# Performance work log

Measured on AMD Instinct MI355X. Metric: run time of the kernel, lower is better.

The kernel has to match this reference:

```python
import jax, jax.numpy as jnp
import numpy as np

HEADS = 8
DIM_HEAD = 64
MP_ADD_T = 0.3
EPS = 1e-4


def normalize_weight(w, eps=EPS):
    # Karras forced weight norm: per-output-channel L2 norm over all other dims
    dims = tuple(range(1, w.ndim))
    n = jnp.sqrt(jnp.sum(w * w, axis=dims, keepdims=True))
    alpha = np.sqrt(n.size / w.size)  # = 1/sqrt(fan_in)
    return w / (eps + alpha * n)


def pixel_norm(t, eps=EPS):
    # F.normalize(dim=-1) * sqrt(d): x / max(||x||, eps) * sqrt(d)
    n = jnp.sqrt(jnp.sum(t * t, axis=-1, keepdims=True))
    return t / jnp.maximum(n, eps) * np.sqrt(t.shape[-1])


def conv1x1(x, w):
    # x: [b,c,h,w], w: [o,c] (normalized weight / sqrt(fan_in))
    wn = normalize_weight(w) / np.sqrt(w.shape[1])  # fan_in = dim_in * 1 * 1
    return jnp.einsum('bchw,oc->bohw', x, wn)


def setup_inputs() -> dict:
    key = jax.random.key(0)
    k1, k2, k3, k4 = jax.random.split(key, 4)
    b, c, h, w = 16, 512, 32, 32
    hidden = HEADS * DIM_HEAD
    return {
        'x': jax.random.normal(k1, (b, c, h, w), dtype=jnp.float32),
        'w_qkv': jax.random.normal(k2, (hidden * 3, c), dtype=jnp.float32),
        'w_out': jax.random.normal(k3, (c, hidden), dtype=jnp.float32),
        'mem_kv': jax.random.normal(k4, (2, HEADS, 4, DIM_HEAD), dtype=jnp.float32),
    }


def reference(x, w_qkv, w_out, mem_kv):
    b, c, h, w = x.shape
    n = h * w
    qkv = conv1x1(x, w_qkv)  # [b, 3*hidden, h, w]
    q, k, v = jnp.split(qkv, 3, axis=1)

    def to_heads(t):
        # b (h c) x y -> b h (x y) c
        return t.reshape(b, HEADS, DIM_HEAD, n).transpose(0, 1, 3, 2)

    q, k, v = map(to_heads, (q, k, v))
    mk = jnp.broadcast_to(mem_kv[0], (b,) + mem_kv[0].shape)  # [b,h,m,d]
    mv = jnp.broadcast_to(mem_kv[1], (b,) + mem_kv[1].shape)
    k = jnp.concatenate([mk, k], axis=2)
    v = jnp.concatenate([mv, v], axis=2)

    q, k, v = map(pixel_norm, (q, k, v))

    sim = jnp.einsum('bhid,bhjd->bhij', q, k) * (DIM_HEAD ** -0.5)
    attn = jax.nn.softmax(sim, axis=-1)  # dropout is identity in eval
    out = jnp.einsum('bhij,bhjd->bhid', attn, v)  # [b,h,n,d]

    # b h (x y) d -> b (h d) x y
    out = out.transpose(0, 1, 3, 2).reshape(b, HEADS * DIM_HEAD, h, w)
    out = conv1x1(out, w_out)

    # MPAdd: magnitude-preserving residual
    t = MP_ADD_T
    den = np.sqrt((1 - t) ** 2 + t ** 2)
    return (out * (1.0 - t) + x * t) / den
```

## Files before the change

kernel.cpp:

```cpp
#include <hip/hip_runtime.h>
#include <hip/hip_bf16.h>
#include <math.h>

#define HEADS 8
#define DIMH 64
#define NPIX 1024
#define BATCH 16
#define CIN 512
#define HIDDEN 512
#define OQKV 1536

typedef __attribute__((ext_vector_type(8))) short v8s;
typedef __attribute__((ext_vector_type(4))) float v4f;
typedef __attribute__((ext_vector_type(4))) int v4i;

#define MFMA16(a, b, c) __builtin_amdgcn_mfma_f32_16x16x32_bf16(a, b, c, 0, 0, 0)

__device__ inline unsigned pkbf(float lo, float hi) {
    unsigned r;
    asm("v_cvt_pk_bf16_f32 %0, %1, %2" : "=v"(r) : "v"(lo), "v"(hi));
    return r;
}
__device__ inline ushort bf16u(float f) {
    __hip_bfloat16 h = __float2bfloat16(f);
    return *(ushort*)&h;
}
__device__ inline float exp2i(float x) {
    float r;
    asm("v_exp_f32 %0, %1" : "=v"(r) : "v"(x));
    return r;
}
__device__ inline float bf2f(ushort u) {
    return __uint_as_float(((unsigned)u) << 16);
}
__device__ inline void gload16(const ushort* g, ushort* l) {
    __builtin_amdgcn_global_load_lds(
        (const __attribute__((address_space(1))) void*)g,
        (__attribute__((address_space(3))) void*)l, 16, 0, 0);
}

#define INVLN2 1.44269504088896f
#define BIAS2  12.2629078475662f

__global__ __launch_bounds__(256) void prep_fused(
    const float* __restrict__ x,
    const float* __restrict__ wq, const float* __restrict__ wo,
    const float* __restrict__ mem_kv,
    ushort* __restrict__ Xt, ushort* __restrict__ wn,
    __hip_bfloat16* __restrict__ mk, __hip_bfloat16* __restrict__ mv,
    float* __restrict__ msk)
{
    int bid = blockIdx.x;
    if (bid < 2048) {
        int b = bid >> 7, rem = bid & 127;
        int c0 = (rem >> 4) * 64, p0 = (rem & 15) * 64;
        __shared__ ushort lds[64][72];
        int tid = threadIdx.x;
        int cl = tid >> 2;
        int pl = (tid & 3) * 16;
        const float* src = x + ((size_t)b * CIN + c0 + cl) * NPIX + p0 + pl;
        #pragma unroll
        for (int j = 0; j < 4; j++) {
            float4 v = *(const float4*)(src + j * 4);
            lds[cl][pl + j * 4 + 0] = bf16u(v.x);
            lds[cl][pl + j * 4 + 1] = bf16u(v.y);
            lds[cl][pl + j * 4 + 2] = bf16u(v.z);
            lds[cl][pl + j * 4 + 3] = bf16u(v.w);
        }
        __syncthreads();
        int pw = tid >> 2;
        int cs = (tid & 3) * 16;
        union { ushort u[16]; uint4 q[2]; } tmp;
        #pragma unroll
        for (int j = 0; j < 16; j++) tmp.u[j] = lds[cs + j][pw];
        ushort* dst = Xt + ((size_t)b * NPIX + p0 + pw) * CIN + c0 + cs;
        *(uint4*)(dst) = tmp.q[0];
        *(uint4*)(dst + 8) = tmp.q[1];
    } else if (bid < 4096) {
        int row = bid - 2048;
        const float* src = (row < OQKV) ? (wq + (size_t)row * CIN)
                                        : (wo + (size_t)(row - OQKV) * CIN);
        int t = threadIdx.x;
        float v0 = src[t];
        float v1 = src[t + 256];
        float ss = v0 * v0 + v1 * v1;
        #pragma unroll
        for (int off = 32; off >= 1; off >>= 1) ss += __shfl_xor(ss, off);
        __shared__ float red[4];
        if ((t & 63) == 0) red[t >> 6] = ss;
        __syncthreads();
        float total = red[0] + red[1] + red[2] + red[3];
        const float RSQRT512 = 0.044194173824159216f;
        const float SQRT512  = 22.627416997969522f;
        float scale = 1.0f / ((1e-4f + sqrtf(total) * RSQRT512) * SQRT512);
        ushort* dst = wn + (size_t)row * CIN;
        dst[t] = bf16u(v0 * scale);
        dst[t + 256] = bf16u(v1 * scale);
    } else {
        if (threadIdx.x < 64) {
            int h = bid - 4096;
            int lane = threadIdx.x;
            #pragma unroll
            for (int m = 0; m < 4; m++) {
                float kvv = mem_kv[((size_t)h * 4 + m) * 64 + lane];
                float vvv = mem_kv[((size_t)(HEADS + h) * 4 + m) * 64 + lane];
                float ssk = kvv * kvv, ssv = vvv * vvv;
                #pragma unroll
                for (int off = 32; off >= 1; off >>= 1) {
                    ssk += __shfl_xor(ssk, off);
                    ssv += __shfl_xor(ssv, off);
                }
                float sck = 8.0f / fmaxf(sqrtf(ssk), 1e-4f);
                float scv = 8.0f / fmaxf(sqrtf(ssv), 1e-4f);
                mk[((size_t)h * 16 + m) * 64 + lane] = __float2bfloat16(kvv);
                mv[((size_t)h * 64 + lane) * 32 + m] = __float2bfloat16(vvv * scv);
                if (lane == 0) { msk[h * 16 + m] = sck; }
            }
            #pragma unroll
            for (int m = 4; m < 16; m++)
                mk[((size_t)h * 16 + m) * 64 + lane] = __float2bfloat16(0.f);
            #pragma unroll
            for (int m = 4; m < 32; m++)
                mv[((size_t)h * 64 + lane) * 32 + m] = __float2bfloat16(0.f);
            if (lane >= 4 && lane < 16) msk[h * 16 + lane] = 0.f;
        }
    }
}

__global__ __launch_bounds__(256) void gemm_qkv_mfma(
    const ushort* __restrict__ Wall,
    const ushort* __restrict__ Xt,
    ushort* __restrict__ Qb, ushort* __restrict__ Kb, ushort* __restrict__ Vb,
    float* __restrict__ qsA)
{
    int bid = blockIdx.x;
    int xcd = bid & 7;
    int rest = bid >> 3;
    int bh2 = rest / 96;
    int r = rest - bh2 * 96;
    int b = xcd + (bh2 << 3);
    int yy = r % 12;
    int pp = r / 12;

    int p0 = pp * 128;
    int isV = (yy >= 8) ? 1 : 0;
    int o0 = (isV ? (yy - 8) : yy) * 128;
    const ushort* Wsrc = Wall + (isV ? (size_t)1024 * CIN : 0);

    int tid = threadIdx.x;
    int wave = tid >> 6, lane = tid & 63;
    int wy = wave >> 1, wx = wave & 1;
    int col = lane & 15, lg = lane >> 4;
    int pw = p0 + wx * 64;
    int ow = o0 + wy * 64;

    __shared__ __align__(16) ushort sW[128 * 64];
    __shared__ __align__(16) ushort sX[128 * 64];

    int rIn = lane >> 3;
    int chS = (lane & 7) ^ rIn;
    int rowStage = wave * 32 + rIn;
    const ushort* gW = Wsrc + (size_t)(o0 + rowStage) * CIN + chS * 8;
    const ushort* gX = Xt + ((size_t)b * NPIX + p0 + rowStage) * CIN + chS * 8;

    v4f acc[4][4];
    #pragma unroll
    for (int i = 0; i < 4; i++)
        #pragma unroll
        for (int j = 0; j < 4; j++) acc[i][j] = (v4f){0.f, 0.f, 0.f, 0.f};

    const ushort* sA = isV ? sX : sW;
    const ushort* sB = isV ? sW : sX;
    int rowA = (isV ? wx : wy) * 64 + col;
    int rowB = (isV ? wy : wx) * 64 + col;
    int c7 = col & 7;

    #pragma unroll 1
    for (int c0 = 0; c0 < CIN; c0 += 64) {
        #pragma unroll
        for (int j = 0; j < 4; j++) {
            gload16(gW + (size_t)j * 8 * CIN + c0, &sW[(wave * 4 + j) * 512]);
            gload16(gX + (size_t)j * 8 * CIN + c0, &sX[(wave * 4 + j) * 512]);
        }
        __syncthreads();
        #pragma unroll
        for (int hh = 0; hh < 2; hh++) {
            int ch = (hh * 4 + lg) ^ c7;
            v8s af[4], bf[4];
            #pragma unroll
            for (int i = 0; i < 4; i++) {
                af[i] = *(const v8s*)&sA[(rowA + i * 16) * 64 + ch * 8];
                bf[i] = *(const v8s*)&sB[(rowB + i * 16) * 64 + ch * 8];
            }
            #pragma unroll
            for (int i = 0; i < 4; i++)
                #pragma unroll
                for (int j = 0; j < 4; j++)
                    acc[i][j] = MFMA16(af[i], bf[j], acc[i][j]);
        }
        __syncthreads();
    }

    if (!isV) {
        int part = ow >> 9;
        int h = (ow >> 6) & 7;
        int bh = b * HEADS + h;

        float ssq[4];
        #pragma unroll
        for (int pt = 0; pt < 4; pt++) {
            float s = 0.f;
            #pragma unroll
            for (int dt = 0; dt < 4; dt++)
                #pragma unroll
                for (int r2 = 0; r2 < 4; r2++) s += acc[dt][pt][r2] * acc[dt][pt][r2];
            s += __shfl_xor(s, 16);
            s += __shfl_xor(s, 32);
            ssq[pt] = s;
        }
        if (part == 0) {
            if (lg == 0) {
                #pragma unroll
                for (int pt = 0; pt < 4; pt++)
                    qsA[(size_t)bh * NPIX + pw + pt * 16 + col] =
                        1.0f / fmaxf(sqrtf(ssq[pt]), 1e-4f);
            }
            ushort* dst = Qb + (size_t)bh * NPIX * DIMH;
            #pragma unroll
            for (int pt = 0; pt < 4; pt++) {
                int p = pw + pt * 16 + col;
                #pragma unroll
                for (int dt = 0; dt < 4; dt++) {
                    uint2 uu;
                    uu.x = pkbf(acc[dt][pt][0], acc[dt][pt][1]);
                    uu.y = pkbf(acc[dt][pt][2], acc[dt][pt][3]);
                    *(uint2*)(dst + (size_t)p * DIMH + dt * 16 + 4 * lg) = uu;
                }
            }
        } else {
            float scl[4];
            #pragma unroll
            for (int pt = 0; pt < 4; pt++)
                scl[pt] = 8.0f / fmaxf(sqrtf(ssq[pt]), 1e-4f);
            ushort* dst = Kb + (size_t)bh * NPIX * DIMH;
            #pragma unroll
            for (int pt = 0; pt < 4; pt++) {
                int p = pw + pt * 16 + col;
                #pragma unroll
                for (int dt = 0; dt < 4; dt++) {
                    uint2 uu;
                    uu.x = pkbf(acc[dt][pt][0] * scl[pt], acc[dt][pt][1] * scl[pt]);
                    uu.y = pkbf(acc[dt][pt][2] * scl[pt], acc[dt][pt][3] * scl[pt]);
                    *(uint2*)(dst + (size_t)p * DIMH + dt * 16 + 4 * lg) = uu;
                }
            }
        }
    } else {
        int h = (ow >> 6) & 7;
        int bh = b * HEADS + h;

        float scl[4][4];
        #pragma unroll
        for (int pt = 0; pt < 4; pt++) {
            #pragma unroll
            for (int r2 = 0; r2 < 4; r2++) {
                float s = acc[pt][0][r2] * acc[pt][0][r2] + acc[pt][1][r2] * acc[pt][1][r2]
                        + acc[pt][2][r2] * acc[pt][2][r2] + acc[pt][3][r2] * acc[pt][3][r2];
                s += __shfl_xor(s, 1);
                s += __shfl_xor(s, 2);
                s += __shfl_xor(s, 4);
                s += __shfl_xor(s, 8);
                scl[pt][r2] = 8.0f / fmaxf(sqrtf(s), 1e-4f);
            }
        }
        #pragma unroll
        for (int ot = 0; ot < 4; ot++) {
            int d = ot * 16 + col;
            #pragma unroll
            for (int pt = 0; pt < 4; pt++) {
                uint2 uu;
                uu.x = pkbf(acc[pt][ot][0] * scl[pt][0], acc[pt][ot][1] * scl[pt][1]);
                uu.y = pkbf(acc[pt][ot][2] * scl[pt][2], acc[pt][ot][3] * scl[pt][3]);
                *(uint2*)(Vb + ((size_t)bh * DIMH + d) * NPIX + pw + pt * 16 + 4 * lg) = uu;
            }
        }
    }
}

__global__ __launch_bounds__(256, 2) void attn_mfma_kernel(
    const __hip_bfloat16* __restrict__ Qb,
    const __hip_bfloat16* __restrict__ Kb,
    const __hip_bfloat16* __restrict__ Vb,
    const float* __restrict__ qsA,
    const __hip_bfloat16* __restrict__ mk, const __hip_bfloat16* __restrict__ mv,
    const float* __restrict__ msk,
    ushort* __restrict__ oP, float* __restrict__ lP)
{
    int bid = blockIdx.x;
    int ks = bid >> 9;
    int bh = bid & 127;
    int qb = (bid >> 7) & 3;
    int b = bh >> 3, h = bh & 7;
    int wave = threadIdx.x >> 6, lane = threadIdx.x & 63;
    int col = lane & 15, lg = lane >> 4;
    int q0 = qb * 256 + wave * 64;

    const __hip_bfloat16* Qbase = Qb + ((size_t)bh * NPIX + q0) * DIMH;
    const __hip_bfloat16* Kbase = Kb + ((size_t)bh * NPIX + ks * 512) * DIMH;
    const __hip_bfloat16* Vbase = Vb + (size_t)bh * DIMH * NPIX + ks * 512;

    v8s qf[4][2];
    float myqs[4];
    #pragma unroll
    for (int qt = 0; qt < 4; qt++) {
        #pragma unroll
        for (int dh = 0; dh < 2; dh++)
            qf[qt][dh] = *(const v8s*)(Qbase + (qt * 16 + col) * DIMH + dh * 32 + 8 * lg);
        myqs[qt] = qsA[(size_t)bh * NPIX + q0 + qt * 16 + col] * INVLN2;
    }

    v4f o_[4][4];
    #pragma unroll
    for (int qt = 0; qt < 4; qt++)
        #pragma unroll
        for (int dt = 0; dt < 4; dt++) o_[qt][dt] = (v4f){0.f, 0.f, 0.f, 0.f};
    float l_[4] = {0.f, 0.f, 0.f, 0.f};

    int srcA = ((lg & 1) << 5) + col;
    int srcB = srcA + 16;
    bool hig = (lg >= 2);

    if (ks == 0) {
        const __hip_bfloat16* mkh = mk + (size_t)h * 16 * DIMH;
        v8s kf0 = *(const v8s*)(mkh + col * DIMH + 8 * lg);
        v8s kf1 = *(const v8s*)(mkh + col * DIMH + 32 + 8 * lg);
        v8s vfm[4];
        #pragma unroll
        for (int dt = 0; dt < 4; dt++)
            vfm[dt] = *(const v8s*)(mv + ((size_t)h * DIMH + dt * 16 + col) * 32 + 8 * lg);
        float4 ksm = *(const float4*)&msk[h * 16 + 4 * lg];
        float ksr[4] = {ksm.x, ksm.y, ksm.z, ksm.w};

        #pragma unroll
        for (int qt = 0; qt < 4; qt++) {
            v4f c0 = (v4f){0.f, 0.f, 0.f, 0.f};
            c0 = MFMA16(kf0, qf[qt][0], c0);
            c0 = MFMA16(kf1, qf[qt][1], c0);
            float p0[4];
            #pragma unroll
            for (int r = 0; r < 4; r++) {
                float t = __builtin_fmaf(c0[r], myqs[qt] * ksr[r], -BIAS2);
                p0[r] = (lg == 0) ? exp2i(t) : 0.f;
                l_[qt] += p0[r];
            }
            unsigned A0 = pkbf(p0[0], p0[1]);
            unsigned A1 = pkbf(p0[2], p0[3]);
            int a0 = __shfl((int)A0, srcA), a1 = __shfl((int)A1, srcA);
            int a2 = __shfl((int)A0, srcB), a3 = __shfl((int)A1, srcB);
            v4i w;
            w.x = hig ? 0 : a0; w.y = hig ? 0 : a1;
            w.z = hig ? 0 : a2; w.w = hig ? 0 : a3;
            v8s pf = __builtin_bit_cast(v8s, w);
            #pragma unroll
            for (int dt = 0; dt < 4; dt++)
                o_[qt][dt] = MFMA16(vfm[dt], pf, o_[qt][dt]);
        }
    }

    v8s kfA[4], vfA[4], kfB[4], vfB[4];

    #define LOADK(dst, kk) { \
        const __hip_bfloat16* Kr = Kbase + (size_t)(kk) * DIMH; \
        dst[0] = *(const v8s*)(Kr + col * DIMH + 8 * lg); \
        dst[1] = *(const v8s*)(Kr + col * DIMH + 32 + 8 * lg); \
        dst[2] = *(const v8s*)(Kr + (16 + col) * DIMH + 8 * lg); \
        dst[3] = *(const v8s*)(Kr + (16 + col) * DIMH + 32 + 8 * lg); }
    #define LOADV(dst, kk) { \
        _Pragma("unroll") \
        for (int dt = 0; dt < 4; dt++) \
            dst[dt] = *(const v8s*)(Vbase + (size_t)(dt * 16 + col) * NPIX + (kk) + 8 * lg); }

    #define COMPUTE(kf, vf) { \
        _Pragma("unroll") \
        for (int qt = 0; qt < 4; qt++) { \
            v4f c0 = (v4f){0.f, 0.f, 0.f, 0.f}; \
            v4f c1 = (v4f){0.f, 0.f, 0.f, 0.f}; \
            __builtin_amdgcn_s_setprio(1); \
            c0 = MFMA16(kf[0], qf[qt][0], c0); \
            c0 = MFMA16(kf[1], qf[qt][1], c0); \
            c1 = MFMA16(kf[2], qf[qt][0], c1); \
            c1 = MFMA16(kf[3], qf[qt][1], c1); \
            __builtin_amdgcn_s_setprio(0); \
            float p0[4], p1[4]; \
            _Pragma("unroll") \
            for (int r = 0; r < 4; r++) { \
                p0[r] = exp2i(__builtin_fmaf(c0[r], myqs[qt], -BIAS2)); \
                p1[r] = exp2i(__builtin_fmaf(c1[r], myqs[qt], -BIAS2)); \
                l_[qt] += p0[r] + p1[r]; \
            } \
            unsigned A0 = pkbf(p0[0], p0[1]); \
            unsigned A1 = pkbf(p0[2], p0[3]); \
            unsigned B0 = pkbf(p1[0], p1[1]); \
            unsigned B1 = pkbf(p1[2], p1[3]); \
            int a0 = __shfl((int)A0, srcA), a1 = __shfl((int)A1, srcA); \
            int a2 = __shfl((int)A0, srcB), a3 = __shfl((int)A1, srcB); \
            int b0 = __shfl((int)B0, srcA), b1 = __shfl((int)B1, srcA); \
            int b2 = __shfl((int)B0, srcB), b3 = __shfl((int)B1, srcB); \
            v4i w; \
            w.x = hig ? b0 : a0; w.y = hig ? b1 : a1; \
            w.z = hig ? b2 : a2; w.w = hig ? b3 : a3; \
            v8s pf = __builtin_bit_cast(v8s, w); \
            __builtin_amdgcn_s_setprio(1); \
            _Pragma("unroll") \
            for (int dt = 0; dt < 4; dt++) \
                o_[qt][dt] = MFMA16(vf[dt], pf, o_[qt][dt]); \
            __builtin_amdgcn_s_setprio(0); \
        } }

    LOADK(kfA, 0);
    LOADV(vfA, 0);
    #pragma unroll 1
    for (int k0 = 0; k0 < 512; k0 += 64) {
        LOADK(kfB, k0 + 32);
        LOADV(vfB, k0 + 32);
        COMPUTE(kfA, vfA);
        LOADK(kfA, k0 + 64);
        LOADV(vfA, k0 + 64);
        COMPUTE(kfB, vfB);
    }

    #pragma unroll
    for (int qt = 0; qt < 4; qt++) {
        float l = l_[qt];
        l += __shfl_xor(l, 16);
        l += __shfl_xor(l, 32);
        int q = q0 + qt * 16 + col;
        if (lg == 0)
            lP[((size_t)ks * 128 + bh) * NPIX + q] = l;
        ushort* od = oP + (((size_t)ks * 128 + bh) * NPIX + q) * DIMH;
        #pragma unroll
        for (int dt = 0; dt < 4; dt++) {
            uint2 uu;
            uu.x = pkbf(o_[qt][dt][0], o_[qt][dt][1]);
            uu.y = pkbf(o_[qt][dt][2], o_[qt][dt][3]);
            *(uint2*)(od + dt * 16 + 4 * lg) = uu;
        }
    }
    #undef LOADK
    #undef LOADV
    #undef COMPUTE
}

__global__ __launch_bounds__(256) void attn_combine(
    const ushort* __restrict__ oP, const float* __restrict__ lP,
    ushort* __restrict__ attT)
{
    int gt = blockIdx.x * 256 + threadIdx.x;
    int rq = gt >> 3;
    int d0 = (gt & 7) * 8;
    int bh = rq >> 10, q = rq & 1023;
    float inv = 1.0f / (lP[rq] + lP[(size_t)128 * NPIX + rq]);
    const ushort* o0p = oP + (size_t)rq * DIMH + d0;
    const ushort* o1p = o0p + (size_t)128 * NPIX * DIMH;
    v8s a = *(const v8s*)o0p;
    v8s c = *(const v8s*)o1p;
    uint4 res;
    unsigned w[4];
    #pragma unroll
    for (int j = 0; j < 4; j++) {
        float lo = (bf2f(((ushort)a[2 * j]))     + bf2f(((ushort)c[2 * j])))     * inv;
        float hi = (bf2f(((ushort)a[2 * j + 1])) + bf2f(((ushort)c[2 * j + 1]))) * inv;
        w[j] = pkbf(lo, hi);
    }
    res.x = w[0]; res.y = w[1]; res.z = w[2]; res.w = w[3];
    int b = bh >> 3, h = bh & 7;
    *(uint4*)(attT + ((size_t)(b * NPIX + q)) * HIDDEN + h * DIMH + d0) = res;
}

__global__ __launch_bounds__(256) void gemm_out_mfma(
    const ushort* __restrict__ Wo,
    const ushort* __restrict__ attT,
    const float* __restrict__ x, float* __restrict__ out)
{
    int b = blockIdx.z;
    int o0 = blockIdx.y * 128;
    int p0 = blockIdx.x * 128;
    int tid = threadIdx.x;
    int wave = tid >> 6, lane = tid & 63;
    int wy = wave >> 1, wx = wave & 1;
    int col = lane & 15, lg = lane >> 4;
    int ow = o0 + wy * 64, pw = p0 + wx * 64;

    __shared__ __align__(16) ushort sAa[128 * 64];
    __shared__ __align__(16) ushort sBb[128 * 64];

    int rIn = lane >> 3;
    int chS = (lane & 7) ^ rIn;
    int rowStage = wave * 32 + rIn;
    const ushort* gA = attT + ((size_t)b * NPIX + p0 + rowStage) * HIDDEN + chS * 8;
    const ushort* gB = Wo + (size_t)(o0 + rowStage) * HIDDEN + chS * 8;

    v4f acc[4][4];
    #pragma unroll
    for (int i = 0; i < 4; i++)
        #pragma unroll
        for (int j = 0; j < 4; j++) acc[i][j] = (v4f){0.f, 0.f, 0.f, 0.f};

    int rowA = wx * 64 + col;
    int rowB = wy * 64 + col;
    int c7 = col & 7;

    #pragma unroll 1
    for (int c0 = 0; c0 < HIDDEN; c0 += 64) {
        #pragma unroll
        for (int j = 0; j < 4; j++) {
            gload16(gA + (size_t)j * 8 * HIDDEN + c0, &sAa[(wave * 4 + j) * 512]);
            gload16(gB + (size_t)j * 8 * HIDDEN + c0, &sBb[(wave * 4 + j) * 512]);
        }
        __syncthreads();
        #pragma unroll
        for (int hh = 0; hh < 2; hh++) {
            int ch = (hh * 4 + lg) ^ c7;
            v8s af[4], bf[4];
            #pragma unroll
            for (int i = 0; i < 4; i++) {
                af[i] = *(const v8s*)&sAa[(rowA + i * 16) * 64 + ch * 8];
                bf[i] = *(const v8s*)&sBb[(rowB + i * 16) * 64 + ch * 8];
            }
            #pragma unroll
            for (int i = 0; i < 4; i++)
                #pragma unroll
                for (int j = 0; j < 4; j++)
                    acc[i][j] = MFMA16(af[i], bf[j], acc[i][j]);
        }
        __syncthreads();
    }

    const float INV_DEN = 1.3130643285972254f;
    #pragma unroll
    for (int pt = 0; pt < 4; pt++) {
        #pragma unroll
        for (int ot = 0; ot < 4; ot++) {
            size_t base = ((size_t)b * HIDDEN + ow + ot * 16 + col) * NPIX
                        + pw + pt * 16 + 4 * lg;
            float4 res = *(const float4*)&x[base];
            float4 y;
            y.x = (acc[pt][ot][0] * 0.7f + res.x * 0.3f) * INV_DEN;
            y.y = (acc[pt][ot][1] * 0.7f + res.y * 0.3f) * INV_DEN;
            y.z = (acc[pt][ot][2] * 0.7f + res.z * 0.3f) * INV_DEN;
            y.w = (acc[pt][ot][3] * 0.7f + res.w * 0.3f) * INV_DEN;
            *(float4*)&out[base] = y;
        }
    }
}

extern "C" void kernel_launch(void* const* d_in, const int* in_sizes, int n_in,
                              void* d_out, int out_size, void* d_ws, size_t ws_size,
                              hipStream_t stream)
{
    const float* x      = (const float*)d_in[0];
    const float* w_qkv  = (const float*)d_in[1];
    const float* w_out  = (const float*)d_in[2];
    const float* mem_kv = (const float*)d_in[3];
    float* out = (float*)d_out;

    char* ws = (char*)d_ws;
    ushort* wnB = (ushort*)ws; ws += (size_t)2048 * CIN * 2;
    ushort* Xt  = (ushort*)ws; ws += (size_t)BATCH * NPIX * CIN * 2;
    ushort* Qb  = (ushort*)ws; ws += (size_t)BATCH * HEADS * NPIX * DIMH * 2;
    ushort* Kb  = (ushort*)ws; ws += (size_t)BATCH * HEADS * NPIX * DIMH * 2;
    ushort* Vb  = (ushort*)ws; ws += (size_t)BATCH * HEADS * NPIX * DIMH * 2;
    ushort* attT = (ushort*)ws; ws += (size_t)BATCH * NPIX * HIDDEN * 2;
    ushort* oP  = (ushort*)ws; ws += (size_t)2 * 128 * NPIX * DIMH * 2;
    float* lP  = (float*)ws;  ws += (size_t)2 * 128 * NPIX * 4;
    float* qsA = (float*)ws;  ws += (size_t)BATCH * HEADS * NPIX * 4;
    float* msk = (float*)ws;  ws += 8 * 16 * 4;
    __hip_bfloat16* mk = (__hip_bfloat16*)ws; ws += (size_t)8 * 16 * 64 * 2;
    __hip_bfloat16* mv = (__hip_bfloat16*)ws; ws += (size_t)8 * 64 * 32 * 2;

    prep_fused<<<4104, 256, 0, stream>>>(
        x, w_qkv, w_out, mem_kv, Xt, wnB, mk, mv, msk);

    gemm_qkv_mfma<<<1536, 256, 0, stream>>>(
        wnB, Xt, Qb, Kb, Vb, qsA);

    attn_mfma_kernel<<<1024, 256, 0, stream>>>(
        (const __hip_bfloat16*)Qb, (const __hip_bfloat16*)Kb,
        (const __hip_bfloat16*)Vb, qsA, mk, mv, msk, oP, lP);

    attn_combine<<<4096, 256, 0, stream>>>(oP, lP, attT);

    gemm_out_mfma<<<dim3(8, 4, BATCH), 256, 0, stream>>>(
        wnB + (size_t)OQKV * CIN, attT, x, out);
}
```

Baseline: 169.6 us.

## Stage K/V tiles through double-buffered swizzled LDS in attention kernel

Each wave previously loaded its own K and V fragments straight from global memory, so the four waves of a block fetched the same K/V data redundantly. Now the block cooperatively copies 64-key tiles of K and V into double-buffered shared memory with an XOR swizzle (via gload16, likely direct global-to-LDS) and prefetches the next tile while computing on the current one. This cuts global/L2 traffic by sharing tiles across waves, at the cost of 32KB of LDS per block, a block barrier per tile, and LDS read latency, which may limit occupancy.

```diff
diff --git a/kernel.cpp b/kernel.cpp
--- a/kernel.cpp
+++ b/kernel.cpp
@@ -305,9 +305,15 @@
     int col = lane & 15, lg = lane >> 4;
     int q0 = qb * 256 + wave * 64;
 
+    __shared__ __align__(16) ushort sK[2][64 * 64];
+    __shared__ __align__(16) ushort sV[2][64 * 64];
+
+    const ushort* Kg = (const ushort*)Kb + ((size_t)bh * NPIX + ks * 512) * DIMH;
+    const ushort* Vg = (const ushort*)Vb + (size_t)bh * DIMH * NPIX + ks * 512;
     const __hip_bfloat16* Qbase = Qb + ((size_t)bh * NPIX + q0) * DIMH;
-    const __hip_bfloat16* Kbase = Kb + ((size_t)bh * NPIX + ks * 512) * DIMH;
-    const __hip_bfloat16* Vbase = Vb + (size_t)bh * DIMH * NPIX + ks * 512;
+
+    int rIn = lane >> 3;
+    int chS = (lane & 7) ^ rIn;
 
     v8s qf[4][2];
     float myqs[4];
@@ -367,20 +373,26 @@
         }
     }
 
-    v8s kfA[4], vfA[4], kfB[4], vfB[4];
-
-    #define LOADK(dst, kk) { \
-        const __hip_bfloat16* Kr = Kbase + (size_t)(kk) * DIMH; \
-        dst[0] = *(const v8s*)(Kr + col * DIMH + 8 * lg); \
-        dst[1] = *(const v8s*)(Kr + col * DIMH + 32 + 8 * lg); \
-        dst[2] = *(const v8s*)(Kr + (16 + col) * DIMH + 8 * lg); \
-        dst[3] = *(const v8s*)(Kr + (16 + col) * DIMH + 32 + 8 * lg); }
-    #define LOADV(dst, kk) { \
+    #define STAGE(cur, kk) { \
+        _Pragma("unroll") \
+        for (int j = 0; j < 2; j++) { \
+            gload16(Kg + ((size_t)(kk) + wave * 16 + j * 8 + rIn) * 64 + chS * 8, \
+                    &sK[cur][wave * 1024 + j * 512]); \
+            gload16(Vg + ((size_t)(wave * 16 + j * 8 + rIn)) * 1024 + (kk) + chS * 8, \
+                    &sV[cur][wave * 1024 + j * 512]); \
+        } }
+
+    #define COMPUTE_LDS(cur, hs) { \
+        v8s kf[4], vf[4]; \
+        int rk0 = (hs) * 32 + col, rk1 = rk0 + 16; \
+        int sw = col & 7; \
+        kf[0] = *(const v8s*)&sK[cur][rk0 * 64 + ((lg    ) ^ sw) * 8]; \
+        kf[1] = *(const v8s*)&sK[cur][rk0 * 64 + ((lg + 4) ^ sw) * 8]; \
+        kf[2] = *(const v8s*)&sK[cur][rk1 * 64 + ((lg    ) ^ sw) * 8]; \
+        kf[3] = *(const v8s*)&sK[cur][rk1 * 64 + ((lg + 4) ^ sw) * 8]; \
         _Pragma("unroll") \
         for (int dt = 0; dt < 4; dt++) \
-            dst[dt] = *(const v8s*)(Vbase + (size_t)(dt * 16 + col) * NPIX + (kk) + 8 * lg); }
-
-    #define COMPUTE(kf, vf) { \
+            vf[dt] = *(const v8s*)&sV[cur][(dt * 16 + col) * 64 + (((hs) * 4 + lg) ^ sw) * 8]; \
         _Pragma("unroll") \
         for (int qt = 0; qt < 4; qt++) { \
             v4f c0 = (v4f){0.f, 0.f, 0.f, 0.f}; \
@@ -417,16 +429,16 @@
             __builtin_amdgcn_s_setprio(0); \
         } }
 
-    LOADK(kfA, 0);
-    LOADV(vfA, 0);
+    int cur = 0;
+    STAGE(0, 0);
+    __syncthreads();
     #pragma unroll 1
-    for (int k0 = 0; k0 < 512; k0 += 64) {
-        LOADK(kfB, k0 + 32);
-        LOADV(vfB, k0 + 32);
-        COMPUTE(kfA, vfA);
-        LOADK(kfA, k0 + 64);
-        LOADV(vfA, k0 + 64);
-        COMPUTE(kfB, vfB);
+    for (int t = 0; t < 8; t++) {
+        if (t < 7) STAGE(cur ^ 1, (t + 1) * 64);
+        COMPUTE_LDS(cur, 0);
+        COMPUTE_LDS(cur, 1);
+        __syncthreads();
+        cur ^= 1;
     }
 
     #pragma unroll
@@ -446,9 +458,8 @@
             *(uint2*)(od + dt * 16 + 4 * lg) = uu;
         }
     }
-    #undef LOADK
-    #undef LOADV
-    #undef COMPUTE
+    #undef STAGE
+    #undef COMPUTE_LDS
 }
 
 __global__ __launch_bounds__(256) void attn_combine(
```

Result: faster. 155.6 us (-8.3%).
